# Kernel tuning notes

Measured on AMD Instinct MI355X. Metric: run time of the kernel, lower is better.

The kernel has to match this reference:

```python
import jax, jax.numpy as jnp
import numpy as np

D_MODEL = 1024  # scale uses full model dim, as in the source
MASKED = True


def setup_inputs() -> dict:
    key = jax.random.key(0)
    kq, kk, kv = jax.random.split(key, 3)
    B, H, S, Dh = 4, 16, 2048, 64
    Q = jax.random.normal(kq, (B, H, S, Dh), dtype=jnp.float32)
    K = jax.random.normal(kk, (B, H, S, Dh), dtype=jnp.float32)
    V = jax.random.normal(kv, (B, H, S, Dh), dtype=jnp.float32)
    return {"Q": Q, "K": K, "V": V}


def reference(Q, K, V):
    scale = 1.0 / (D_MODEL ** 0.5)
    # [B,H,Sq,Sk] score matrix
    scores = jnp.einsum('bhqd,bhkd->bhqk', Q, K) * scale
    if MASKED:
        S = Q.shape[-2]
        causal = jnp.tril(jnp.ones((S, S), dtype=bool))  # True on/below diag
        scores = jnp.where(causal, scores, jnp.float32(-jnp.inf))
    probs = jax.nn.softmax(scores, axis=-1)
    return jnp.einsum('bhqk,bhkd->bhqd', probs, V)
```

## Files before the change

### kernel.cpp

```cpp
#include <hip/hip_runtime.h>

typedef _Float16 half2_t __attribute__((ext_vector_type(2)));
typedef _Float16 half4_t __attribute__((ext_vector_type(4)));
typedef _Float16 half8_t __attribute__((ext_vector_type(8)));
typedef float    f32x4   __attribute__((ext_vector_type(4)));
typedef unsigned int u32x4 __attribute__((ext_vector_type(4)));

#define S_LEN 2048
#define DH    64
#define QBLK  128
#define KVB   64
#define NQB   16
#define SCALE 0.045110910340389066f
#define DEFER_THR 8.0f

__device__ __forceinline__ int swz_off(int row, int byteInRow) {
    return row * 128 + (byteInRow ^ ((row & 7) << 4));
}

__device__ __forceinline__ half4_t cvt4(f32x4 x) {
    half2_t a = __builtin_bit_cast(half2_t, __builtin_amdgcn_cvt_pkrtz(x[0], x[1]));
    half2_t b = __builtin_bit_cast(half2_t, __builtin_amdgcn_cvt_pkrtz(x[2], x[3]));
    half4_t r; r[0] = a[0]; r[1] = a[1]; r[2] = b[0]; r[3] = b[1];
    return r;
}
__device__ __forceinline__ unsigned int pk2(float a, float b) {
    return __builtin_bit_cast(unsigned int, __builtin_amdgcn_cvt_pkrtz(a, b));
}
__device__ __forceinline__ float fmax3(float a, float b, float c) {
    return fmaxf(fmaxf(a, b), c);
}

__global__ __launch_bounds__(512, 4)
void fattn_kernel(const float* __restrict__ Qg, const float* __restrict__ Kg,
                  const float* __restrict__ Vg, float* __restrict__ Og) {
    __shared__ __align__(16) char smem[32768];

    const int bh  = (int)blockIdx.x;
    const int qb  = (NQB - 1) - (int)blockIdx.y;
    const int q0  = qb * QBLK;
    const int tid = (int)threadIdx.x;
    const int lane = tid & 63;
    const int w    = tid >> 6;
    const int c    = lane & 15;
    const int g    = lane >> 4;

    const size_t base = (size_t)bh * S_LEN * DH;
    const float* Qp = Qg + base;
    const float* Kp = Kg + base;
    const float* Vp = Vg + base;
    float*       Op = Og + base;

    const int qrow = q0 + w * 16;
    const int nT = 2 * qb + 2;

    const bool isK = tid < 256;
    const int sid = tid & 255;
    const int r0  = sid >> 4;
    const int c4  = (sid & 15) << 2;
    const int kLds0 = swz_off(r0, c4 * 2);
    const int kq4 = (sid >> 4) << 2;
    const int d4  = (sid & 15) << 2;
    const int kqc = kq4 & 31;
    const int vColByte = ((kqc < 16) ? (4 * kqc) : (4 * kqc - 56)) + ((kq4 & 32) << 1);

    half8_t qf0, qf1;
    {
        const float* qptr = Qp + (size_t)(qrow + c) * DH;
#pragma unroll
        for (int s = 0; s < 2; ++s) {
            f32x4 a = *(const f32x4*)(qptr + s * 32 + g * 8);
            f32x4 b = *(const f32x4*)(qptr + s * 32 + g * 8 + 4);
            half8_t h;
#pragma unroll
            for (int j = 0; j < 4; ++j) {
                h[j]     = (_Float16)(a[j] * SCALE);
                h[j + 4] = (_Float16)(b[j] * SCALE);
            }
            if (s == 0) qf0 = h; else qf1 = h;
        }
    }

    f32x4 oacc[4];
#pragma unroll
    for (int dt = 0; dt < 4; ++dt) oacc[dt] = (f32x4){0.f, 0.f, 0.f, 0.f};
    float nm = 0.f;
    float l_run = 0.f;

    f32x4 pr[4];
    auto stage_load = [&](int kv) {
        if (isK) {
#pragma unroll
            for (int i = 0; i < 4; ++i)
                pr[i] = *(const f32x4*)(Kp + (size_t)((kv + r0 + 16 * i) * DH + c4));
        } else {
#pragma unroll
            for (int j = 0; j < 4; ++j)
                pr[j] = *(const f32x4*)(Vp + (size_t)((kv + kq4 + j) * DH + d4));
        }
    };
    auto stage_write = [&](char* buf) {
        if (isK) {
#pragma unroll
            for (int i = 0; i < 4; ++i)
                *(half4_t*)(buf + kLds0 + i * 2048) = cvt4(pr[i]);
        } else {
            char* Vw = buf + 8192;
#pragma unroll
            for (int jj = 0; jj < 4; ++jj) {
                half2_t lo = __builtin_bit_cast(half2_t, __builtin_amdgcn_cvt_pkrtz(pr[0][jj], pr[1][jj]));
                half2_t hi = __builtin_bit_cast(half2_t, __builtin_amdgcn_cvt_pkrtz(pr[2][jj], pr[3][jj]));
                half4_t col; col[0] = lo[0]; col[1] = lo[1]; col[2] = hi[0]; col[3] = hi[1];
                *(half4_t*)(Vw + swz_off(d4 + jj, vColByte)) = col;
            }
        }
    };

    stage_load(0);
    stage_write(smem);

    int cur = 0;
    for (int t = 0; t < nT; ++t) {
        __syncthreads();
        const bool pf = (t + 1 < nT);
        if (pf) stage_load((t + 1) * KVB);

        const int kv0 = t * KVB;
        char* const Ks = smem + cur * 16384;
        char* const Vs = Ks + 8192;

        if (kv0 <= qrow + 15) {
            f32x4 st[4];
#pragma unroll
            for (int kt = 0; kt < 4; ++kt) st[kt] = (f32x4){nm, nm, nm, nm};
            __builtin_amdgcn_s_setprio(1);
#pragma unroll
            for (int kt = 0; kt < 4; ++kt) {
                half8_t kf0 = *(const half8_t*)(Ks + swz_off(kt * 16 + c, g * 16));
                half8_t kf1 = *(const half8_t*)(Ks + swz_off(kt * 16 + c, 64 + g * 16));
                st[kt] = __builtin_amdgcn_mfma_f32_16x16x32_f16(kf0, qf0, st[kt], 0, 0, 0);
                st[kt] = __builtin_amdgcn_mfma_f32_16x16x32_f16(kf1, qf1, st[kt], 0, 0, 0);
            }
            __builtin_amdgcn_s_setprio(0);

            if (kv0 + KVB - 1 > qrow) {
                const int qq = qrow + c;
#pragma unroll
                for (int kt = 0; kt < 4; ++kt)
#pragma unroll
                    for (int r = 0; r < 4; ++r)
                        if (kv0 + kt * 16 + g * 4 + r > qq) st[kt][r] = -1e30f;
            }

            float m0 = fmax3(st[0][0], st[0][1], st[0][2]);
            float m1 = fmax3(st[0][3], st[1][0], st[1][1]);
            float m2 = fmax3(st[1][2], st[1][3], st[2][0]);
            float m3 = fmax3(st[2][1], st[2][2], st[2][3]);
            float m4 = fmax3(st[3][0], st[3][1], st[3][2]);
            float tmax = fmaxf(fmax3(fmax3(m0, m1, m2), m3, m4), st[3][3]);
            if (!__all(tmax <= DEFER_THR)) {
                float tr = fmaxf(tmax, __shfl_xor(tmax, 16));
                tr = fmaxf(tr, __shfl_xor(tr, 32));
                const float delta = fmaxf(tr, 0.f);
                const float alpha = __builtin_amdgcn_exp2f(-delta);
                nm -= delta;
                l_run *= alpha;
#pragma unroll
                for (int dt = 0; dt < 4; ++dt) oacc[dt] = oacc[dt] * alpha;
#pragma unroll
                for (int kt = 0; kt < 4; ++kt) st[kt] = st[kt] - delta;
            }
            float tsum = 0.f;
            unsigned int pw[8];
#pragma unroll
            for (int kt = 0; kt < 4; ++kt) {
#pragma unroll
                for (int r = 0; r < 4; ++r) {
                    float p = __builtin_amdgcn_exp2f(st[kt][r]);
                    tsum += p;
                    st[kt][r] = p;
                }
                pw[2 * kt]     = pk2(st[kt][0], st[kt][1]);
                pw[2 * kt + 1] = pk2(st[kt][2], st[kt][3]);
            }
            l_run += tsum;
            const half8_t ph0 = __builtin_bit_cast(half8_t, (u32x4){pw[0], pw[1], pw[2], pw[3]});
            const half8_t ph1 = __builtin_bit_cast(half8_t, (u32x4){pw[4], pw[5], pw[6], pw[7]});

            __builtin_amdgcn_s_setprio(1);
#pragma unroll
            for (int dt = 0; dt < 4; ++dt) {
                half8_t vf = *(const half8_t*)(Vs + swz_off(dt * 16 + c, g * 16));
                oacc[dt] = __builtin_amdgcn_mfma_f32_16x16x32_f16(vf, ph0, oacc[dt], 0, 0, 0);
            }
#pragma unroll
            for (int dt = 0; dt < 4; ++dt) {
                half8_t vf = *(const half8_t*)(Vs + swz_off(dt * 16 + c, 64 + g * 16));
                oacc[dt] = __builtin_amdgcn_mfma_f32_16x16x32_f16(vf, ph1, oacc[dt], 0, 0, 0);
            }
            __builtin_amdgcn_s_setprio(0);
        }

        if (pf) stage_write(smem + (cur ^ 1) * 16384);
        cur ^= 1;
    }

    l_run += __shfl_xor(l_run, 16);
    l_run += __shfl_xor(l_run, 32);
    const float inv = __builtin_amdgcn_rcpf(l_run);
    float* optr = Op + (size_t)(qrow + c) * DH;
#pragma unroll
    for (int dt = 0; dt < 4; ++dt) {
        f32x4 o = oacc[dt] * inv;
        *(f32x4*)(optr + dt * 16 + g * 4) = o;
    }
}

extern "C" void kernel_launch(void* const* d_in, const int* in_sizes, int n_in,
                              void* d_out, int out_size, void* d_ws, size_t ws_size,
                              hipStream_t stream) {
    (void)in_sizes; (void)n_in; (void)out_size; (void)d_ws; (void)ws_size;
    const float* Q = (const float*)d_in[0];
    const float* K = (const float*)d_in[1];
    const float* V = (const float*)d_in[2];
    float* O = (float*)d_out;
    dim3 grid(64, NQB);
    fattn_kernel<<<grid, 512, 0, stream>>>(Q, K, V, O);
}
```

Measured before the change: 67.38 us.

## Split long causal query blocks across two KV halves with combine kernel

Query blocks 8-15 are now split into two work units that each cover half of the KV range. A constant table schedules units in longest-first order, and each partial unit writes its unnormalized output, running max and sum to workspace. A second kernel merges the two partials with log-sum-exp weights. The aim is to even out the causal load imbalance and add parallelism, at the cost of extra workspace traffic, a second launch, and a fallback path whose blocks exit early when the workspace is too small.

```diff
diff --git a/kernel.cpp b/kernel.cpp
--- a/kernel.cpp
+++ b/kernel.cpp
@@ -14,6 +14,14 @@
 #define SCALE 0.045110910340389066f
 #define DEFER_THR 8.0f
 
+#define CHUNK_F32 8448
+#define WS_NEED   (1024u * CHUNK_F32 * 4u)
+
+__constant__ unsigned char UNITS[24] = {
+    0x1F, 0x2F, 0x07, 0x1E, 0x2E, 0x06, 0x1D, 0x2D,
+    0x1C, 0x2C, 0x05, 0x1B, 0x2B, 0x1A, 0x2A, 0x04,
+    0x19, 0x29, 0x18, 0x28, 0x03, 0x02, 0x01, 0x00 };
+
 __device__ __forceinline__ int swz_off(int row, int byteInRow) {
     return row * 128 + (byteInRow ^ ((row & 7) << 4));
 }
@@ -33,11 +41,25 @@
 
 __global__ __launch_bounds__(512, 4)
 void fattn_kernel(const float* __restrict__ Qg, const float* __restrict__ Kg,
-                  const float* __restrict__ Vg, float* __restrict__ Og) {
+                  const float* __restrict__ Vg, float* __restrict__ Og,
+                  float* __restrict__ ws, int split) {
     __shared__ __align__(16) char smem[32768];
 
-    const int bh  = (int)blockIdx.x;
-    const int qb  = (NQB - 1) - (int)blockIdx.y;
+    const int bh = (int)blockIdx.x;
+    const unsigned u = UNITS[blockIdx.y];
+    const int qb   = u & 15;
+    const int type = u >> 4;
+    int t0, t1, partial;
+    if (split) {
+        partial = (type != 0);
+        t0 = (type == 2) ? (qb + 1) : 0;
+        t1 = (type == 1) ? (qb + 1) : (2 * qb + 2);
+    } else {
+        if (type == 2) return;
+        partial = 0;
+        t0 = 0; t1 = 2 * qb + 2;
+    }
+
     const int q0  = qb * QBLK;
     const int tid = (int)threadIdx.x;
     const int lane = tid & 63;
@@ -52,7 +74,6 @@
     float*       Op = Og + base;
 
     const int qrow = q0 + w * 16;
-    const int nT = 2 * qb + 2;
 
     const bool isK = tid < 256;
     const int sid = tid & 255;
@@ -116,13 +137,13 @@
         }
     };
 
-    stage_load(0);
+    stage_load(t0 * KVB);
     stage_write(smem);
 
     int cur = 0;
-    for (int t = 0; t < nT; ++t) {
+    for (int t = t0; t < t1; ++t) {
         __syncthreads();
-        const bool pf = (t + 1 < nT);
+        const bool pf = (t + 1 < t1);
         if (pf) stage_load((t + 1) * KVB);
 
         const int kv0 = t * KVB;
@@ -207,23 +228,71 @@
 
     l_run += __shfl_xor(l_run, 16);
     l_run += __shfl_xor(l_run, 32);
-    const float inv = __builtin_amdgcn_rcpf(l_run);
-    float* optr = Op + (size_t)(qrow + c) * DH;
-#pragma unroll
-    for (int dt = 0; dt < 4; ++dt) {
-        f32x4 o = oacc[dt] * inv;
-        *(f32x4*)(optr + dt * 16 + g * 4) = o;
+    if (!partial) {
+        const float inv = __builtin_amdgcn_rcpf(l_run);
+        float* optr = Op + (size_t)(qrow + c) * DH;
+#pragma unroll
+        for (int dt = 0; dt < 4; ++dt) {
+            f32x4 o = oacc[dt] * inv;
+            *(f32x4*)(optr + dt * 16 + g * 4) = o;
+        }
+    } else {
+        float* wsp = ws + (size_t)(((bh << 3) + (qb - 8)) * 2 + (type - 1)) * CHUNK_F32;
+        const int row = w * 16 + c;
+        float* optr = wsp + row * 64;
+#pragma unroll
+        for (int dt = 0; dt < 4; ++dt)
+            *(f32x4*)(optr + dt * 16 + g * 4) = oacc[dt];
+        if (g == 0) {
+            wsp[8192 + row] = nm;
+            wsp[8320 + row] = l_run;
+        }
+    }
+}
+
+__global__ __launch_bounds__(256)
+void combine_kernel(const float* __restrict__ ws, float* __restrict__ Og) {
+    const int bh  = (int)blockIdx.x;
+    const int qbi = (int)blockIdx.y;
+    const float* p0 = ws + (size_t)((bh * 8 + qbi) * 2) * CHUNK_F32;
+    const float* p1 = p0 + CHUNK_F32;
+    __shared__ float c0s[128], c1s[128];
+    const int t = (int)threadIdx.x;
+    if (t < 128) {
+        float a0 = -p0[8192 + t], l0 = p0[8320 + t];
+        float a1 = -p1[8192 + t], l1 = p1[8320 + t];
+        float M  = fmaxf(a0, a1);
+        float w0 = exp2f(a0 - M), w1 = exp2f(a1 - M);
+        float inv = 1.0f / (w0 * l0 + w1 * l1);
+        c0s[t] = w0 * inv;
+        c1s[t] = w1 * inv;
+    }
+    __syncthreads();
+    float* Op = Og + ((size_t)bh * S_LEN + 1024 + qbi * 128) * DH;
+#pragma unroll 2
+    for (int i = t; i < 2048; i += 256) {
+        const int row = i >> 4;
+        f32x4 o0 = *(const f32x4*)(p0 + i * 4);
+        f32x4 o1 = *(const f32x4*)(p1 + i * 4);
+        f32x4 o  = o0 * c0s[row] + o1 * c1s[row];
+        *(f32x4*)(Op + i * 4) = o;
     }
 }
 
 extern "C" void kernel_launch(void* const* d_in, const int* in_sizes, int n_in,
                               void* d_out, int out_size, void* d_ws, size_t ws_size,
                               hipStream_t stream) {
-    (void)in_sizes; (void)n_in; (void)out_size; (void)d_ws; (void)ws_size;
+    (void)in_sizes; (void)n_in; (void)out_size;
     const float* Q = (const float*)d_in[0];
     const float* K = (const float*)d_in[1];
     const float* V = (const float*)d_in[2];
-    float* O = (float*)d_out;
-    dim3 grid(64, NQB);
-    fattn_kernel<<<grid, 512, 0, stream>>>(Q, K, V, O);
-}
+    float* O  = (float*)d_out;
+    float* ws = (float*)d_ws;
+    const int split = (ws_size >= (size_t)WS_NEED) ? 1 : 0;
+    dim3 grid(64, 24);
+    fattn_kernel<<<grid, 512, 0, stream>>>(Q, K, V, O, ws, split);
+    if (split) {
+        dim3 cg(64, 8);
+        combine_kernel<<<cg, 256, 0, stream>>>(ws, O);
+    }
+}
```

New measurement: 76.98 us. 14.3% more time.

## Process two 16-row query tiles per wave with 256-thread blocks

Applied to the files above, without the earlier changes.

Halves the block to 4 waves, with each wave handling 32 query rows as two 16-row MFMA tiles. Each K/V fragment read from LDS now feeds twice as many MFMAs, and each staging thread loads 8 rows instead of 4. This is meant to cut LDS traffic per FLOP and the block-level sync overhead. In exchange it raises register pressure (two accumulator sets and 8 prefetch registers) and leaves fewer waves per block to hide latency.

```diff
diff --git a/kernel.cpp b/kernel.cpp
--- a/kernel.cpp
+++ b/kernel.cpp
@@ -31,7 +31,7 @@
     return fmaxf(fmaxf(a, b), c);
 }
 
-__global__ __launch_bounds__(512, 4)
+__global__ __launch_bounds__(256, 3)
 void fattn_kernel(const float* __restrict__ Qg, const float* __restrict__ Kg,
                   const float* __restrict__ Vg, float* __restrict__ Og) {
     __shared__ __align__(16) char smem[32768];
@@ -51,22 +51,22 @@
     const float* Vp = Vg + base;
     float*       Op = Og + base;
 
-    const int qrow = q0 + w * 16;
+    const int qrow = q0 + w * 32;
     const int nT = 2 * qb + 2;
 
-    const bool isK = tid < 256;
-    const int sid = tid & 255;
+    const bool isK = tid < 128;
+    const int sid = tid & 127;
     const int r0  = sid >> 4;
     const int c4  = (sid & 15) << 2;
     const int kLds0 = swz_off(r0, c4 * 2);
     const int kq4 = (sid >> 4) << 2;
     const int d4  = (sid & 15) << 2;
-    const int kqc = kq4 & 31;
-    const int vColByte = ((kqc < 16) ? (4 * kqc) : (4 * kqc - 56)) + ((kq4 & 32) << 1);
-
-    half8_t qf0, qf1;
-    {
-        const float* qptr = Qp + (size_t)(qrow + c) * DH;
+    const int vb = (kq4 < 16) ? (4 * kq4) : (4 * kq4 - 56);
+
+    half8_t qf[2][2];
+#pragma unroll
+    for (int qt = 0; qt < 2; ++qt) {
+        const float* qptr = Qp + (size_t)(qrow + qt * 16 + c) * DH;
 #pragma unroll
         for (int s = 0; s < 2; ++s) {
             f32x4 a = *(const f32x4*)(qptr + s * 32 + g * 8);
@@ -77,42 +77,49 @@
                 h[j]     = (_Float16)(a[j] * SCALE);
                 h[j + 4] = (_Float16)(b[j] * SCALE);
             }
-            if (s == 0) qf0 = h; else qf1 = h;
-        }
-    }
-
-    f32x4 oacc[4];
-#pragma unroll
-    for (int dt = 0; dt < 4; ++dt) oacc[dt] = (f32x4){0.f, 0.f, 0.f, 0.f};
-    float nm = 0.f;
-    float l_run = 0.f;
-
-    f32x4 pr[4];
+            qf[qt][s] = h;
+        }
+    }
+
+    f32x4 oacc0[4], oacc1[4];
+#pragma unroll
+    for (int dt = 0; dt < 4; ++dt) {
+        oacc0[dt] = (f32x4){0.f, 0.f, 0.f, 0.f};
+        oacc1[dt] = (f32x4){0.f, 0.f, 0.f, 0.f};
+    }
+    float nm0 = 0.f, nm1 = 0.f;
+    float l0 = 0.f, l1 = 0.f;
+
+    f32x4 pr[8];
     auto stage_load = [&](int kv) {
         if (isK) {
 #pragma unroll
-            for (int i = 0; i < 4; ++i)
-                pr[i] = *(const f32x4*)(Kp + (size_t)((kv + r0 + 16 * i) * DH + c4));
+            for (int i = 0; i < 8; ++i)
+                pr[i] = *(const f32x4*)(Kp + (size_t)((kv + r0 + 8 * i) * DH + c4));
         } else {
 #pragma unroll
-            for (int j = 0; j < 4; ++j)
-                pr[j] = *(const f32x4*)(Vp + (size_t)((kv + kq4 + j) * DH + d4));
+            for (int h = 0; h < 2; ++h)
+#pragma unroll
+                for (int j = 0; j < 4; ++j)
+                    pr[4 * h + j] = *(const f32x4*)(Vp + (size_t)((kv + kq4 + 32 * h + j) * DH + d4));
         }
     };
     auto stage_write = [&](char* buf) {
         if (isK) {
 #pragma unroll
-            for (int i = 0; i < 4; ++i)
-                *(half4_t*)(buf + kLds0 + i * 2048) = cvt4(pr[i]);
+            for (int i = 0; i < 8; ++i)
+                *(half4_t*)(buf + kLds0 + i * 1024) = cvt4(pr[i]);
         } else {
             char* Vw = buf + 8192;
 #pragma unroll
-            for (int jj = 0; jj < 4; ++jj) {
-                half2_t lo = __builtin_bit_cast(half2_t, __builtin_amdgcn_cvt_pkrtz(pr[0][jj], pr[1][jj]));
-                half2_t hi = __builtin_bit_cast(half2_t, __builtin_amdgcn_cvt_pkrtz(pr[2][jj], pr[3][jj]));
-                half4_t col; col[0] = lo[0]; col[1] = lo[1]; col[2] = hi[0]; col[3] = hi[1];
-                *(half4_t*)(Vw + swz_off(d4 + jj, vColByte)) = col;
-            }
+            for (int h = 0; h < 2; ++h)
+#pragma unroll
+                for (int jj = 0; jj < 4; ++jj) {
+                    half2_t lo = __builtin_bit_cast(half2_t, __builtin_amdgcn_cvt_pkrtz(pr[4*h+0][jj], pr[4*h+1][jj]));
+                    half2_t hi = __builtin_bit_cast(half2_t, __builtin_amdgcn_cvt_pkrtz(pr[4*h+2][jj], pr[4*h+3][jj]));
+                    half4_t col; col[0] = lo[0]; col[1] = lo[1]; col[2] = hi[0]; col[3] = hi[1];
+                    *(half4_t*)(Vw + swz_off(d4 + jj, vb + 64 * h)) = col;
+                }
         }
     };
 
@@ -129,74 +136,122 @@
         char* const Ks = smem + cur * 16384;
         char* const Vs = Ks + 8192;
 
-        if (kv0 <= qrow + 15) {
-            f32x4 st[4];
-#pragma unroll
-            for (int kt = 0; kt < 4; ++kt) st[kt] = (f32x4){nm, nm, nm, nm};
+        if (kv0 <= qrow + 31) {
+            f32x4 st0[4], st1[4];
+#pragma unroll
+            for (int kt = 0; kt < 4; ++kt) {
+                st0[kt] = (f32x4){nm0, nm0, nm0, nm0};
+                st1[kt] = (f32x4){nm1, nm1, nm1, nm1};
+            }
             __builtin_amdgcn_s_setprio(1);
 #pragma unroll
             for (int kt = 0; kt < 4; ++kt) {
                 half8_t kf0 = *(const half8_t*)(Ks + swz_off(kt * 16 + c, g * 16));
                 half8_t kf1 = *(const half8_t*)(Ks + swz_off(kt * 16 + c, 64 + g * 16));
-                st[kt] = __builtin_amdgcn_mfma_f32_16x16x32_f16(kf0, qf0, st[kt], 0, 0, 0);
-                st[kt] = __builtin_amdgcn_mfma_f32_16x16x32_f16(kf1, qf1, st[kt], 0, 0, 0);
+                st0[kt] = __builtin_amdgcn_mfma_f32_16x16x32_f16(kf0, qf[0][0], st0[kt], 0, 0, 0);
+                st0[kt] = __builtin_amdgcn_mfma_f32_16x16x32_f16(kf1, qf[0][1], st0[kt], 0, 0, 0);
+                st1[kt] = __builtin_amdgcn_mfma_f32_16x16x32_f16(kf0, qf[1][0], st1[kt], 0, 0, 0);
+                st1[kt] = __builtin_amdgcn_mfma_f32_16x16x32_f16(kf1, qf[1][1], st1[kt], 0, 0, 0);
             }
             __builtin_amdgcn_s_setprio(0);
 
             if (kv0 + KVB - 1 > qrow) {
-                const int qq = qrow + c;
+                const int qq0 = qrow + c;
+                const int qq1 = qrow + 16 + c;
 #pragma unroll
                 for (int kt = 0; kt < 4; ++kt)
 #pragma unroll
-                    for (int r = 0; r < 4; ++r)
-                        if (kv0 + kt * 16 + g * 4 + r > qq) st[kt][r] = -1e30f;
-            }
-
-            float m0 = fmax3(st[0][0], st[0][1], st[0][2]);
-            float m1 = fmax3(st[0][3], st[1][0], st[1][1]);
-            float m2 = fmax3(st[1][2], st[1][3], st[2][0]);
-            float m3 = fmax3(st[2][1], st[2][2], st[2][3]);
-            float m4 = fmax3(st[3][0], st[3][1], st[3][2]);
-            float tmax = fmaxf(fmax3(fmax3(m0, m1, m2), m3, m4), st[3][3]);
-            if (!__all(tmax <= DEFER_THR)) {
-                float tr = fmaxf(tmax, __shfl_xor(tmax, 16));
-                tr = fmaxf(tr, __shfl_xor(tr, 32));
-                const float delta = fmaxf(tr, 0.f);
-                const float alpha = __builtin_amdgcn_exp2f(-delta);
-                nm -= delta;
-                l_run *= alpha;
-#pragma unroll
-                for (int dt = 0; dt < 4; ++dt) oacc[dt] = oacc[dt] * alpha;
-#pragma unroll
-                for (int kt = 0; kt < 4; ++kt) st[kt] = st[kt] - delta;
-            }
-            float tsum = 0.f;
+                    for (int r = 0; r < 4; ++r) {
+                        const int kk = kv0 + kt * 16 + g * 4 + r;
+                        if (kk > qq0) st0[kt][r] = -1e30f;
+                        if (kk > qq1) st1[kt][r] = -1e30f;
+                    }
+            }
+
             unsigned int pw[8];
-#pragma unroll
-            for (int kt = 0; kt < 4; ++kt) {
-#pragma unroll
-                for (int r = 0; r < 4; ++r) {
-                    float p = __builtin_amdgcn_exp2f(st[kt][r]);
-                    tsum += p;
-                    st[kt][r] = p;
-                }
-                pw[2 * kt]     = pk2(st[kt][0], st[kt][1]);
-                pw[2 * kt + 1] = pk2(st[kt][2], st[kt][3]);
-            }
-            l_run += tsum;
-            const half8_t ph0 = __builtin_bit_cast(half8_t, (u32x4){pw[0], pw[1], pw[2], pw[3]});
-            const half8_t ph1 = __builtin_bit_cast(half8_t, (u32x4){pw[4], pw[5], pw[6], pw[7]});
+            {
+                float m0 = fmax3(st0[0][0], st0[0][1], st0[0][2]);
+                float m1 = fmax3(st0[0][3], st0[1][0], st0[1][1]);
+                float m2 = fmax3(st0[1][2], st0[1][3], st0[2][0]);
+                float m3 = fmax3(st0[2][1], st0[2][2], st0[2][3]);
+                float m4 = fmax3(st0[3][0], st0[3][1], st0[3][2]);
+                float tmax = fmaxf(fmax3(fmax3(m0, m1, m2), m3, m4), st0[3][3]);
+                if (!__all(tmax <= DEFER_THR)) {
+                    float tr = fmaxf(tmax, __shfl_xor(tmax, 16));
+                    tr = fmaxf(tr, __shfl_xor(tr, 32));
+                    const float delta = fmaxf(tr, 0.f);
+                    const float alpha = __builtin_amdgcn_exp2f(-delta);
+                    nm0 -= delta;
+                    l0 *= alpha;
+#pragma unroll
+                    for (int dt = 0; dt < 4; ++dt) oacc0[dt] = oacc0[dt] * alpha;
+#pragma unroll
+                    for (int kt = 0; kt < 4; ++kt) st0[kt] = st0[kt] - delta;
+                }
+                float tsum = 0.f;
+#pragma unroll
+                for (int kt = 0; kt < 4; ++kt) {
+#pragma unroll
+                    for (int r = 0; r < 4; ++r) {
+                        float p = __builtin_amdgcn_exp2f(st0[kt][r]);
+                        tsum += p;
+                        st0[kt][r] = p;
+                    }
+                    pw[2 * kt]     = pk2(st0[kt][0], st0[kt][1]);
+                    pw[2 * kt + 1] = pk2(st0[kt][2], st0[kt][3]);
+                }
+                l0 += tsum;
+            }
+            const half8_t phA0 = __builtin_bit_cast(half8_t, (u32x4){pw[0], pw[1], pw[2], pw[3]});
+            const half8_t phA1 = __builtin_bit_cast(half8_t, (u32x4){pw[4], pw[5], pw[6], pw[7]});
+            {
+                float m0 = fmax3(st1[0][0], st1[0][1], st1[0][2]);
+                float m1 = fmax3(st1[0][3], st1[1][0], st1[1][1]);
+                float m2 = fmax3(st1[1][2], st1[1][3], st1[2][0]);
+                float m3 = fmax3(st1[2][1], st1[2][2], st1[2][3]);
+                float m4 = fmax3(st1[3][0], st1[3][1], st1[3][2]);
+                float tmax = fmaxf(fmax3(fmax3(m0, m1, m2), m3, m4), st1[3][3]);
+                if (!__all(tmax <= DEFER_THR)) {
+                    float tr = fmaxf(tmax, __shfl_xor(tmax, 16));
+                    tr = fmaxf(tr, __shfl_xor(tr, 32));
+                    const float delta = fmaxf(tr, 0.f);
+                    const float alpha = __builtin_amdgcn_exp2f(-delta);
+                    nm1 -= delta;
+                    l1 *= alpha;
+#pragma unroll
+                    for (int dt = 0; dt < 4; ++dt) oacc1[dt] = oacc1[dt] * alpha;
+#pragma unroll
+                    for (int kt = 0; kt < 4; ++kt) st1[kt] = st1[kt] - delta;
+                }
+                float tsum = 0.f;
+#pragma unroll
+                for (int kt = 0; kt < 4; ++kt) {
+#pragma unroll
+                    for (int r = 0; r < 4; ++r) {
+                        float p = __builtin_amdgcn_exp2f(st1[kt][r]);
+                        tsum += p;
+                        st1[kt][r] = p;
+                    }
+                    pw[2 * kt]     = pk2(st1[kt][0], st1[kt][1]);
+                    pw[2 * kt + 1] = pk2(st1[kt][2], st1[kt][3]);
+                }
+                l1 += tsum;
+            }
+            const half8_t phB0 = __builtin_bit_cast(half8_t, (u32x4){pw[0], pw[1], pw[2], pw[3]});
+            const half8_t phB1 = __builtin_bit_cast(half8_t, (u32x4){pw[4], pw[5], pw[6], pw[7]});
 
             __builtin_amdgcn_s_setprio(1);
 #pragma unroll
             for (int dt = 0; dt < 4; ++dt) {
                 half8_t vf = *(const half8_t*)(Vs + swz_off(dt * 16 + c, g * 16));
-                oacc[dt] = __builtin_amdgcn_mfma_f32_16x16x32_f16(vf, ph0, oacc[dt], 0, 0, 0);
+                oacc0[dt] = __builtin_amdgcn_mfma_f32_16x16x32_f16(vf, phA0, oacc0[dt], 0, 0, 0);
+                oacc1[dt] = __builtin_amdgcn_mfma_f32_16x16x32_f16(vf, phB0, oacc1[dt], 0, 0, 0);
             }
 #pragma unroll
             for (int dt = 0; dt < 4; ++dt) {
                 half8_t vf = *(const half8_t*)(Vs + swz_off(dt * 16 + c, 64 + g * 16));
-                oacc[dt] = __builtin_amdgcn_mfma_f32_16x16x32_f16(vf, ph1, oacc[dt], 0, 0, 0);
+                oacc0[dt] = __builtin_amdgcn_mfma_f32_16x16x32_f16(vf, phA1, oacc0[dt], 0, 0, 0);
+                oacc1[dt] = __builtin_amdgcn_mfma_f32_16x16x32_f16(vf, phB1, oacc1[dt], 0, 0, 0);
             }
             __builtin_amdgcn_s_setprio(0);
         }
@@ -205,14 +260,29 @@
         cur ^= 1;
     }
 
-    l_run += __shfl_xor(l_run, 16);
-    l_run += __shfl_xor(l_run, 32);
-    const float inv = __builtin_amdgcn_rcpf(l_run);
-    float* optr = Op + (size_t)(qrow + c) * DH;
-#pragma unroll
-    for (int dt = 0; dt < 4; ++dt) {
-        f32x4 o = oacc[dt] * inv;
-        *(f32x4*)(optr + dt * 16 + g * 4) = o;
+    {
+        float lr = l0;
+        lr += __shfl_xor(lr, 16);
+        lr += __shfl_xor(lr, 32);
+        const float inv = __builtin_amdgcn_rcpf(lr);
+        float* optr = Op + (size_t)(qrow + c) * DH;
+#pragma unroll
+        for (int dt = 0; dt < 4; ++dt) {
+            f32x4 o = oacc0[dt] * inv;
+            *(f32x4*)(optr + dt * 16 + g * 4) = o;
+        }
+    }
+    {
+        float lr = l1;
+        lr += __shfl_xor(lr, 16);
+        lr += __shfl_xor(lr, 32);
+        const float inv = __builtin_amdgcn_rcpf(lr);
+        float* optr = Op + (size_t)(qrow + 16 + c) * DH;
+#pragma unroll
+        for (int dt = 0; dt < 4; ++dt) {
+            f32x4 o = oacc1[dt] * inv;
+            *(f32x4*)(optr + dt * 16 + g * 4) = o;
+        }
     }
 }
 
@@ -225,5 +295,5 @@
     const float* V = (const float*)d_in[2];
     float* O = (float*)d_out;
     dim3 grid(64, NQB);
-    fattn_kernel<<<grid, 512, 0, stream>>>(Q, K, V, O);
-}
+    fattn_kernel<<<grid, 256, 0, stream>>>(Q, K, V, O);
+}
```

After: 60.00 us. -10.9%, faster.
